# Kernel tuning notes

Hardware: AMD Instinct MI355X
Metric: run time of the kernel (lower is better)

Reference implementation:

```python
import jax, jax.numpy as jnp
import numpy as np

K = 16  # knn_k
LN_EPS = 1e-5


def _layernorm(x, g, b):
    mu = jnp.mean(x, axis=-1, keepdims=True)
    var = jnp.var(x, axis=-1, keepdims=True)
    return (x - mu) * jax.lax.rsqrt(var + LN_EPS) * g + b


def _mlp_block(x, W1, b1, g, be, W2, b2):
    # Linear -> LayerNorm -> GELU -> Linear (MLPBlock)
    h = x @ W1 + b1
    h = jax.nn.gelu(_layernorm(h, g, be))
    return h @ W2 + b2


def _knn(v):
    # v: [N,3] -> indices of K nearest neighbors [N,K] (self included, as in knn search)
    sq = jnp.sum(v * v, axis=-1)                       # [N]
    d = sq[:, None] + sq[None, :] - 2.0 * (v @ v.T)    # [N,N] squared dists
    return jax.lax.top_k(-d, K)[1]                     # [N,K]


def setup_inputs() -> dict:
    key = jax.random.key(0)
    ks = jax.random.split(key, 8)
    B, N, C_IN, C_OUT, HID = 2, 8192, 32, 64, 128
    E_IN = C_IN + C_IN + 3  # 67
    s = 0.02
    return {
        "vertices": jax.random.normal(ks[0], (B, N, 3), jnp.float32),
        "features": jax.random.normal(ks[1], (B, N, C_IN), jnp.float32),
        "W1": jax.random.normal(ks[2], (E_IN, HID), jnp.float32) * s,
        "b1": jnp.zeros((HID,), jnp.float32),
        "g1": jnp.ones((HID,), jnp.float32),
        "be1": jnp.zeros((HID,), jnp.float32),
        "W2": jax.random.normal(ks[3], (HID, C_OUT), jnp.float32) * s,
        "b2": jnp.zeros((C_OUT,), jnp.float32),
        "Wo1": jax.random.normal(ks[4], (C_OUT, HID), jnp.float32) * s,
        "bo1": jnp.zeros((HID,), jnp.float32),
        "go": jnp.ones((HID,), jnp.float32),
        "beo": jnp.zeros((HID,), jnp.float32),
        "Wo2": jax.random.normal(ks[5], (HID, C_OUT), jnp.float32) * s,
        "bo2": jnp.zeros((C_OUT,), jnp.float32),
    }


def reference(vertices, features, W1, b1, g1, be1, W2, b2,
              Wo1, bo1, go, beo, Wo2, bo2):
    # out_point_feature_type == 'same': output points == input points
    idx = jax.vmap(_knn)(vertices)                                   # [B,N,K]
    gather = jax.vmap(lambda a, i: jnp.take(a, i, axis=0))
    neigh_feat = gather(features, idx)                               # [B,N,K,C]
    neigh_vert = gather(vertices, idx)                               # [B,N,K,3]
    self_feat = jnp.broadcast_to(features[:, :, None, :], neigh_feat.shape)
    rel_pos = neigh_vert - vertices[:, :, None, :]                   # [B,N,K,3]
    edge = jnp.concatenate([neigh_feat, self_feat, rel_pos], axis=-1)  # [B,N,K,2C+3]
    edge = _mlp_block(edge, W1, b1, g1, be1, W2, b2)                 # [B,N,K,C_out]
    out = jnp.mean(edge, axis=2)                                     # 'mean' reduction over K neighbors
    out = _mlp_block(out, Wo1, bo1, go, beo, Wo2, bo2)               # [B,N,C_out]
    return out
```

## Files before the change

kernel.cpp:

```cpp
#include <hip/hip_runtime.h>
#include <hip/hip_bf16.h>
#include <math.h>

#define BATCH 2
#define NPTS  8192
#define CIN   32
#define HID   128
#define COUT  64
#define EIN   67
#define KNN   16

#define TILE  1024
#define CAP   128
#define CAP2  128

#define G      8
#define GROUPS 4
#define NBLK   (BATCH*NPTS/(G*GROUPS))

typedef unsigned short u16;
typedef unsigned long long u64;
typedef __attribute__((ext_vector_type(8))) short bf16x8;
typedef __attribute__((ext_vector_type(4))) float f32x4;

__device__ __forceinline__ u16 f2b(float f) {
    unsigned u = __float_as_uint(f);
    return (u16)((u + 0x7FFFu + ((u >> 16) & 1u)) >> 16);
}
__device__ __forceinline__ unsigned pk2(float a, float b) {
    return (unsigned)f2b(a) | ((unsigned)f2b(b) << 16);
}
__device__ __forceinline__ float gelu_t(float x) {
    float u = 1.5957691216057308f * (x + 0.044715f * x * x * x);
    float ex = __expf(u);
    return x * ex / (ex + 1.0f);
}

__global__ void prep_kernel(const float* __restrict__ verts, float4* __restrict__ pv) {
    int i = blockIdx.x * blockDim.x + threadIdx.x;
    if (i >= BATCH * NPTS) return;
    float x = verts[3 * i], y = verts[3 * i + 1], z = verts[3 * i + 2];
    float sq = __fadd_rn(__fadd_rn(__fmul_rn(x, x), __fmul_rn(y, y)), __fmul_rn(z, z));
    pv[i] = make_float4(x, y, z, sq);
}

__global__ __launch_bounds__(256, 4) void knn3_kernel(const float4* __restrict__ pv,
                                                      int* __restrict__ nbr_out_rows) {
    __shared__ float4 minv4[4][64];
    __shared__ float bufD[4][4][CAP2];
    __shared__ int   bufJ[4][4][CAP2];

    const int tid = threadIdx.x, lane = tid & 63, wv = tid >> 6;
    const int pt0 = (blockIdx.x * 4 + wv) * 4;
    const int b = pt0 >> 13, i0 = pt0 & (NPTS - 1);
    const float4* P = pv + (size_t)b * NPTS;

    float4 sp[4];
#pragma unroll
    for (int p = 0; p < 4; ++p) sp[p] = P[i0 + p];

    float mn[4] = {INFINITY, INFINITY, INFINITY, INFINITY};
#pragma unroll 4
    for (int t = 0; t < 64; ++t) {
        float4 c = P[t * 64 + lane];
#pragma unroll
        for (int p = 0; p < 4; ++p) {
            float dot = __fmul_rn(sp[p].x, c.x);
            dot = __fmaf_rn(sp[p].y, c.y, dot);
            dot = __fmaf_rn(sp[p].z, c.z, dot);
            float d = __fsub_rn(__fadd_rn(sp[p].w, c.w), __fmul_rn(2.0f, dot));
            mn[p] = fminf(mn[p], d);
        }
    }

    minv4[wv][lane] = make_float4(mn[0], mn[1], mn[2], mn[3]);
    __syncthreads();
    int rk[4] = {0, 0, 0, 0};
    for (int mm = 0; mm < 64; ++mm) {
        float4 v = minv4[wv][mm];
        rk[0] += (v.x < mn[0]) || (v.x == mn[0] && mm < lane);
        rk[1] += (v.y < mn[1]) || (v.y == mn[1] && mm < lane);
        rk[2] += (v.z < mn[2]) || (v.z == mn[2] && mm < lane);
        rk[3] += (v.w < mn[3]) || (v.w == mn[3] && mm < lane);
    }
    float tau[4];
#pragma unroll
    for (int p = 0; p < 4; ++p) {
        u64 bal = __ballot(rk[p] == 15);
        int srcl = __ffsll(bal) - 1;
        tau[p] = __shfl(mn[p], srcl, 64);
    }

    int base[4] = {0, 0, 0, 0};
#pragma unroll 2
    for (int t = 0; t < 128; ++t) {
        float4 c = P[t * 64 + lane];
        int j = t * 64 + lane;
#pragma unroll
        for (int p = 0; p < 4; ++p) {
            float dot = __fmul_rn(sp[p].x, c.x);
            dot = __fmaf_rn(sp[p].y, c.y, dot);
            dot = __fmaf_rn(sp[p].z, c.z, dot);
            float d = __fsub_rn(__fadd_rn(sp[p].w, c.w), __fmul_rn(2.0f, dot));
            bool pred = (d <= tau[p]);
            u64 mk = __ballot(pred);
            if (mk != 0ull) {
                if (pred) {
                    int pos = base[p] + (int)__popcll(mk & ((1ull << lane) - 1ull));
                    if (pos < CAP2) { bufD[wv][p][pos] = d; bufJ[wv][p][pos] = j; }
                }
                base[p] += (int)__popcll(mk);
            }
        }
    }

#pragma unroll
    for (int p = 0; p < 4; ++p) {
        int ns = (base[p] > CAP2) ? CAP2 : base[p];
        for (int slot = 0; slot < 2; ++slot) {
            int sidx = slot * 64 + lane;
            if (sidx < ns) {
                float ds = bufD[wv][p][sidx];
                int   js = bufJ[wv][p][sidx];
                int rank = 0;
                for (int mm = 0; mm < ns; ++mm) {
                    float dm = bufD[wv][p][mm];
                    int   jm = bufJ[wv][p][mm];
                    rank += (dm < ds) || (dm == ds && jm < js);
                }
                if (rank < KNN) nbr_out_rows[(size_t)(pt0 + p) * 64 + rank] = js;
            }
        }
    }
}

__global__ __launch_bounds__(256) void knn_kernel(const float* __restrict__ verts,
                                                  int* nbr_out_rows) {
    __shared__ float4 tilebuf[TILE];
    __shared__ float  bufD[4][CAP];
    __shared__ int    bufJ[4][CAP];

    const int tid = threadIdx.x, lane = tid & 63, wv = tid >> 6;
    const int pt = blockIdx.x * 4 + wv;
    const int b = pt >> 13, i = pt & (NPTS - 1);
    const float* vb = verts + (size_t)b * NPTS * 3;

    const float xi = vb[3 * i], yi = vb[3 * i + 1], zi = vb[3 * i + 2];
    const float sqi = __fadd_rn(__fadd_rn(__fmul_rn(xi, xi), __fmul_rn(yi, yi)),
                                __fmul_rn(zi, zi));

    float m_d = INFINITY;
    for (int t = 0; t < NPTS / TILE; ++t) {
        __syncthreads();
        for (int s = 0; s < TILE / 256; ++s) {
            int p = t * TILE + s * 256 + tid;
            float px = vb[3 * p], py = vb[3 * p + 1], pz = vb[3 * p + 2];
            float sq = __fadd_rn(__fadd_rn(__fmul_rn(px, px), __fmul_rn(py, py)),
                                 __fmul_rn(pz, pz));
            tilebuf[s * 256 + tid] = make_float4(px, py, pz, sq);
        }
        __syncthreads();
        for (int it = 0; it < TILE / 64; ++it) {
            float4 c = tilebuf[it * 64 + lane];
            float dot = __fmul_rn(xi, c.x);
            dot = __fmaf_rn(yi, c.y, dot);
            dot = __fmaf_rn(zi, c.z, dot);
            float d = __fsub_rn(__fadd_rn(sqi, c.w), __fmul_rn(2.0f, dot));
            m_d = fminf(m_d, d);
        }
    }
    __shared__ float minv[4][64];
    minv[wv][lane] = m_d;
    __syncthreads();
    int rnk = 0;
    for (int mm = 0; mm < 64; ++mm) {
        float vm = minv[wv][mm];
        rnk += (vm < m_d) || (vm == m_d && mm < lane);
    }
    u64 bal = __ballot(rnk == 15);
    float tau = __shfl(m_d, __ffsll(bal) - 1, 64);

    int base = 0;
    for (int t = 0; t < NPTS / TILE; ++t) {
        __syncthreads();
        for (int s = 0; s < TILE / 256; ++s) {
            int p = t * TILE + s * 256 + tid;
            float px = vb[3 * p], py = vb[3 * p + 1], pz = vb[3 * p + 2];
            float sq = __fadd_rn(__fadd_rn(__fmul_rn(px, px), __fmul_rn(py, py)),
                                 __fmul_rn(pz, pz));
            tilebuf[s * 256 + tid] = make_float4(px, py, pz, sq);
        }
        __syncthreads();
        for (int it = 0; it < TILE / 64; ++it) {
            int jl = it * 64 + lane;
            float4 c = tilebuf[jl];
            float dot = __fmul_rn(xi, c.x);
            dot = __fmaf_rn(yi, c.y, dot);
            dot = __fmaf_rn(zi, c.z, dot);
            float d = __fsub_rn(__fadd_rn(sqi, c.w), __fmul_rn(2.0f, dot));
            bool pred = (d <= tau);
            u64 mask = __ballot(pred);
            if (pred) {
                int pos = base + (int)__popcll(mask & ((1ull << lane) - 1ull));
                if (pos < CAP) { bufD[wv][pos] = d; bufJ[wv][pos] = t * TILE + jl; }
            }
            base += (int)__popcll(mask);
        }
    }
    int ns = (base > CAP) ? CAP : base;
    __syncthreads();
#pragma unroll
    for (int slot = 0; slot < 2; ++slot) {
        int sidx = slot * 64 + lane;
        if (sidx < ns) {
            float ds = bufD[wv][sidx];
            int   js = bufJ[wv][sidx];
            int rank = 0;
            for (int mm = 0; mm < ns; ++mm) {
                float dm = bufD[wv][mm];
                int   jm = bufJ[wv][mm];
                rank += (dm < ds) || (dm == ds && jm < js);
            }
            if (rank < KNN) nbr_out_rows[(size_t)pt * 64 + rank] = js;
        }
    }
}

__global__ __launch_bounds__(256, 2) void edge_kernel(
    const float* __restrict__ verts, const float* __restrict__ feats,
    const float* __restrict__ W1, const float* __restrict__ b1,
    const float* __restrict__ g1, const float* __restrict__ be1,
    const float* __restrict__ W2, const float* __restrict__ b2,
    const float* __restrict__ Wo1, const float* __restrict__ bo1,
    const float* __restrict__ go_, const float* __restrict__ beo,
    const float* __restrict__ Wo2, const float* __restrict__ bo2,
    float* out)
{
    __shared__ u16 EP[G][4][64][8];
    __shared__ u16 W1F[3][8][64][8];
    __shared__ float b1s[HID], g1s[HID], be1s[HID];
    __shared__ float b2s[COUT];
    __shared__ float meansh[32][68];
    __shared__ int   nbrs[G][KNN];

    const int tid  = threadIdx.x;
    const int lane = tid & 63, wv = tid >> 6;
    const int quad = lane >> 4, n16 = lane & 15;

    for (int s = tid; s < 3 * 8 * 64; s += 256) {
        int kt = s >> 9, nt = (s >> 6) & 7, ln = s & 63;
        int q = ln >> 4, nn = ln & 15;
        int col = nt * 16 + nn;
        union { bf16x8 v; unsigned u[4]; } pk;
#pragma unroll
        for (int jj = 0; jj < 4; ++jj) {
            int k0 = kt * 32 + q * 8 + jj * 2;
            float a  = (k0     < EIN) ? W1[(size_t)k0 * HID + col]       : 0.0f;
            float bq = (k0 + 1 < EIN) ? W1[(size_t)(k0 + 1) * HID + col] : 0.0f;
            pk.u[jj] = pk2(a, bq);
        }
        *(bf16x8*)&W1F[kt][nt][ln][0] = pk.v;
    }
    if (tid < HID) { b1s[tid] = b1[tid]; g1s[tid] = g1[tid]; be1s[tid] = be1[tid]; }
    if (tid < COUT) b2s[tid] = b2[tid];

    bf16x8 w2r[4][4];
#pragma unroll
    for (int kt2 = 0; kt2 < 4; ++kt2)
#pragma unroll
        for (int nt2 = 0; nt2 < 4; ++nt2) {
            union { bf16x8 v; unsigned u[4]; } pk;
#pragma unroll
            for (int jj = 0; jj < 4; ++jj) {
                int k0 = kt2 * 32 + quad * 8 + jj * 2;
                int o = nt2 * 16 + n16;
                pk.u[jj] = pk2(W2[(size_t)k0 * COUT + o],
                               W2[(size_t)(k0 + 1) * COUT + o]);
            }
            w2r[kt2][nt2] = pk.v;
        }

    for (int g = 0; g < GROUPS; ++g) {
        const int P0 = (blockIdx.x * GROUPS + g) * G;
        const int bb = P0 >> 13;
        const float* fb  = feats + (size_t)bb * NPTS * CIN;
        const float* vbk = verts + (size_t)bb * NPTS * 3;

        __syncthreads();
        if (tid < G * KNN)
            nbrs[tid >> 4][tid & 15] =
                ((const int*)out)[(size_t)(P0 + (tid >> 4)) * 64 + (tid & 15)];
        __syncthreads();

        {
            int m = tid & 127;
            int p = m >> 4, k = m & 15;
            int coff = tid >> 7;
            int jn = nbrs[p][k];
            int ip = (P0 & (NPTS - 1)) + p;
#pragma unroll
            for (int it = 0; it < 6; ++it) {
                int c8 = it * 2 + coff;
                union { bf16x8 v; unsigned u[4]; } pk;
                if (c8 < 4) {
                    const float* src = fb + (size_t)jn * CIN + c8 * 8;
                    float4 A = *(const float4*)src, B4 = *(const float4*)(src + 4);
                    pk.u[0] = pk2(A.x, A.y); pk.u[1] = pk2(A.z, A.w);
                    pk.u[2] = pk2(B4.x, B4.y); pk.u[3] = pk2(B4.z, B4.w);
                } else if (c8 < 8) {
                    const float* src = fb + (size_t)ip * CIN + (c8 - 4) * 8;
                    float4 A = *(const float4*)src, B4 = *(const float4*)(src + 4);
                    pk.u[0] = pk2(A.x, A.y); pk.u[1] = pk2(A.z, A.w);
                    pk.u[2] = pk2(B4.x, B4.y); pk.u[3] = pk2(B4.z, B4.w);
                } else if (c8 == 8) {
                    float dx = vbk[3 * jn]     - vbk[3 * ip];
                    float dy = vbk[3 * jn + 1] - vbk[3 * ip + 1];
                    float dz = vbk[3 * jn + 2] - vbk[3 * ip + 2];
                    pk.u[0] = pk2(dx, dy); pk.u[1] = pk2(dz, 0.0f);
                    pk.u[2] = 0u; pk.u[3] = 0u;
                } else {
                    pk.u[0] = pk.u[1] = pk.u[2] = pk.u[3] = 0u;
                }
                *(bf16x8*)&EP[p][c8 >> 2][k + 16 * (c8 & 3)][0] = pk.v;
            }
        }
        __syncthreads();

#pragma unroll
        for (int half = 0; half < 2; ++half) {
            const int mt = wv + half * 4;

            f32x4 acc[8];
#pragma unroll
            for (int nt = 0; nt < 8; ++nt) acc[nt] = (f32x4){0.f, 0.f, 0.f, 0.f};
#pragma unroll
            for (int kt = 0; kt < 3; ++kt) {
                bf16x8 a = *(bf16x8*)&EP[mt][kt][lane][0];
#pragma unroll
                for (int nt = 0; nt < 8; ++nt) {
                    bf16x8 bfr = *(bf16x8*)&W1F[kt][nt][lane][0];
                    acc[nt] = __builtin_amdgcn_mfma_f32_16x16x32_bf16(a, bfr, acc[nt], 0, 0, 0);
                }
            }

            float b1v[8], g1v[8], bev[8];
#pragma unroll
            for (int nt = 0; nt < 8; ++nt) {
                b1v[nt] = b1s[nt * 16 + n16];
                g1v[nt] = g1s[nt * 16 + n16];
                bev[nt] = be1s[nt * 16 + n16];
            }
            float s1[4] = {0,0,0,0}, s2[4] = {0,0,0,0};
#pragma unroll
            for (int nt = 0; nt < 8; ++nt)
#pragma unroll
                for (int r = 0; r < 4; ++r) {
                    float x = acc[nt][r] + b1v[nt];
                    s1[r] += x; s2[r] += x * x;
                }
#pragma unroll
            for (int r = 0; r < 4; ++r) {
#pragma unroll
                for (int off = 1; off < 16; off <<= 1) {
                    s1[r] += __shfl_xor(s1[r], off, 64);
                    s2[r] += __shfl_xor(s2[r], off, 64);
                }
            }
            float mu[4], rs[4];
#pragma unroll
            for (int r = 0; r < 4; ++r) {
                mu[r] = s1[r] * (1.0f / HID);
                float var = s2[r] * (1.0f / HID) - mu[r] * mu[r];
                rs[r] = rsqrtf(var + 1e-5f);
            }

#pragma unroll
            for (int nt = 0; nt < 8; ++nt) {
                int kt2 = nt >> 1;
                int q2  = (nt * 2 + (n16 >> 3)) & 3;
                int jj  = n16 & 7;
#pragma unroll
                for (int r = 0; r < 4; ++r) {
                    float x  = acc[nt][r] + b1v[nt];
                    float xn = (x - mu[r]) * rs[r] * g1v[nt] + bev[nt];
                    EP[mt][kt2][quad * 4 + r + 16 * q2][jj] = (u16)f2b(gelu_t(xn));
                }
            }

            f32x4 acc2[4];
#pragma unroll
            for (int nt2 = 0; nt2 < 4; ++nt2) acc2[nt2] = (f32x4){0.f, 0.f, 0.f, 0.f};
#pragma unroll
            for (int kt2 = 0; kt2 < 4; ++kt2) {
                bf16x8 a2 = *(bf16x8*)&EP[mt][kt2][lane][0];
#pragma unroll
                for (int nt2 = 0; nt2 < 4; ++nt2)
                    acc2[nt2] = __builtin_amdgcn_mfma_f32_16x16x32_bf16(a2, w2r[kt2][nt2], acc2[nt2], 0, 0, 0);
            }

#pragma unroll
            for (int nt2 = 0; nt2 < 4; ++nt2) {
                float cs = acc2[nt2][0] + acc2[nt2][1] + acc2[nt2][2] + acc2[nt2][3];
                cs += __shfl_xor(cs, 16, 64);
                cs += __shfl_xor(cs, 32, 64);
                if (quad == 0) {
                    int o = nt2 * 16 + n16;
                    meansh[g * 8 + mt][o] = cs * (1.0f / KNN) + b2s[o];
                }
            }
        }
    }

    __syncthreads();

    for (int s = tid; s < 2 * 8 * 64; s += 256) {
        int kt = s >> 9, nt = (s >> 6) & 7, ln = s & 63;
        int q = ln >> 4, nn = ln & 15;
        int col = nt * 16 + nn;
        union { bf16x8 v; unsigned u[4]; } pk;
#pragma unroll
        for (int jj = 0; jj < 4; ++jj) {
            int k0 = kt * 32 + q * 8 + jj * 2;
            pk.u[jj] = pk2(Wo1[(size_t)k0 * HID + col],
                           Wo1[(size_t)(k0 + 1) * HID + col]);
        }
        *(bf16x8*)&W1F[kt][nt][ln][0] = pk.v;
    }
    if (tid < HID) { b1s[tid] = bo1[tid]; g1s[tid] = go_[tid]; be1s[tid] = beo[tid]; }
    if (tid < COUT) b2s[tid] = bo2[tid];
#pragma unroll
    for (int kt2 = 0; kt2 < 4; ++kt2)
#pragma unroll
        for (int nt2 = 0; nt2 < 4; ++nt2) {
            union { bf16x8 v; unsigned u[4]; } pk;
#pragma unroll
            for (int jj = 0; jj < 4; ++jj) {
                int k0 = kt2 * 32 + quad * 8 + jj * 2;
                int o = nt2 * 16 + n16;
                pk.u[jj] = pk2(Wo2[(size_t)k0 * COUT + o],
                               Wo2[(size_t)(k0 + 1) * COUT + o]);
            }
            w2r[kt2][nt2] = pk.v;
        }
    __syncthreads();

    if (wv < 2) {
        const int tile = wv;

        bf16x8 af[2];
#pragma unroll
        for (int kt = 0; kt < 2; ++kt) {
            const float* mrow = &meansh[tile * 16 + n16][kt * 32 + quad * 8];
            float4 A = *(const float4*)mrow, B4 = *(const float4*)(mrow + 4);
            union { bf16x8 v; unsigned u[4]; } pk;
            pk.u[0] = pk2(A.x, A.y); pk.u[1] = pk2(A.z, A.w);
            pk.u[2] = pk2(B4.x, B4.y); pk.u[3] = pk2(B4.z, B4.w);
            af[kt] = pk.v;
        }

        f32x4 acc[8];
#pragma unroll
        for (int nt = 0; nt < 8; ++nt) acc[nt] = (f32x4){0.f, 0.f, 0.f, 0.f};
#pragma unroll
        for (int kt = 0; kt < 2; ++kt)
#pragma unroll
            for (int nt = 0; nt < 8; ++nt) {
                bf16x8 bfr = *(bf16x8*)&W1F[kt][nt][lane][0];
                acc[nt] = __builtin_amdgcn_mfma_f32_16x16x32_bf16(af[kt], bfr, acc[nt], 0, 0, 0);
            }

        float b1v[8], g1v[8], bev[8];
#pragma unroll
        for (int nt = 0; nt < 8; ++nt) {
            b1v[nt] = b1s[nt * 16 + n16];
            g1v[nt] = g1s[nt * 16 + n16];
            bev[nt] = be1s[nt * 16 + n16];
        }
        float s1[4] = {0,0,0,0}, s2[4] = {0,0,0,0};
#pragma unroll
        for (int nt = 0; nt < 8; ++nt)
#pragma unroll
            for (int r = 0; r < 4; ++r) {
                float x = acc[nt][r] + b1v[nt];
                s1[r] += x; s2[r] += x * x;
            }
#pragma unroll
        for (int r = 0; r < 4; ++r) {
#pragma unroll
            for (int off = 1; off < 16; off <<= 1) {
                s1[r] += __shfl_xor(s1[r], off, 64);
                s2[r] += __shfl_xor(s2[r], off, 64);
            }
        }
#pragma unroll
        for (int nt = 0; nt < 8; ++nt) {
            int kt2 = nt >> 1;
            int q2  = (nt * 2 + (n16 >> 3)) & 3;
            int jj  = n16 & 7;
#pragma unroll
            for (int r = 0; r < 4; ++r) {
                float mu = s1[r] * (1.0f / HID);
                float var = s2[r] * (1.0f / HID) - mu * mu;
                float rs = rsqrtf(var + 1e-5f);
                float x  = acc[nt][r] + b1v[nt];
                float xn = (x - mu) * rs * g1v[nt] + bev[nt];
                EP[tile][kt2][quad * 4 + r + 16 * q2][jj] = (u16)f2b(gelu_t(xn));
            }
        }

        f32x4 acc2[4];
#pragma unroll
        for (int nt2 = 0; nt2 < 4; ++nt2) acc2[nt2] = (f32x4){0.f, 0.f, 0.f, 0.f};
#pragma unroll
        for (int kt2 = 0; kt2 < 4; ++kt2) {
            bf16x8 a2 = *(bf16x8*)&EP[tile][kt2][lane][0];
#pragma unroll
            for (int nt2 = 0; nt2 < 4; ++nt2)
                acc2[nt2] = __builtin_amdgcn_mfma_f32_16x16x32_bf16(a2, w2r[kt2][nt2], acc2[nt2], 0, 0, 0);
        }

#pragma unroll
        for (int nt2 = 0; nt2 < 4; ++nt2) {
            int o = nt2 * 16 + n16;
#pragma unroll
            for (int r = 0; r < 4; ++r) {
                int ptl = blockIdx.x * 32 + tile * 16 + quad * 4 + r;
                out[(size_t)ptl * 64 + o] = acc2[nt2][r] + b2s[o];
            }
        }
    }
}

extern "C" void kernel_launch(void* const* d_in, const int* in_sizes, int n_in,
                              void* d_out, int out_size, void* d_ws, size_t ws_size,
                              hipStream_t stream) {
    const float* verts = (const float*)d_in[0];
    const float* feats = (const float*)d_in[1];
    const float* W1  = (const float*)d_in[2];
    const float* b1  = (const float*)d_in[3];
    const float* g1  = (const float*)d_in[4];
    const float* be1 = (const float*)d_in[5];
    const float* W2  = (const float*)d_in[6];
    const float* b2  = (const float*)d_in[7];
    const float* Wo1 = (const float*)d_in[8];
    const float* bo1 = (const float*)d_in[9];
    const float* go_ = (const float*)d_in[10];
    const float* beo = (const float*)d_in[11];
    const float* Wo2 = (const float*)d_in[12];
    const float* bo2 = (const float*)d_in[13];
    float* out = (float*)d_out;

    (void)in_sizes; (void)n_in; (void)out_size;

    const size_t pv_bytes = (size_t)BATCH * NPTS * sizeof(float4);
    if (ws_size >= pv_bytes) {
        float4* pv = (float4*)d_ws;
        prep_kernel<<<(BATCH * NPTS + 255) / 256, 256, 0, stream>>>(verts, pv);
        knn3_kernel<<<(BATCH * NPTS) / 16, 256, 0, stream>>>(pv, (int*)out);
    } else {
        knn_kernel<<<(BATCH * NPTS) / 4, 256, 0, stream>>>(verts, (int*)out);
    }
    edge_kernel<<<NBLK, 256, 0, stream>>>(
        verts, feats, W1, b1, g1, be1, W2, b2,
        Wo1, bo1, go_, beo, Wo2, bo2, out);
}
```

Before: 229.0 us.

## Rework KNN to 8 queries per wave and per-wave edge MLP pipeline

The KNN kernel now handles 8 query points per wave and uses a folded FMA form of the distance (-2x·c + |c|^2) with a small margin on the threshold. Candidates are collected through LDS atomics, and exact distances are recomputed only for the selected candidates. The edge kernel is restructured so each wave processes its own 4 points with software-prefetched register loads, replacing block-wide shared gather and sync, and the grid now uses 16 points per block. This trades more KNN registers and lower occupancy, plus nondeterministic candidate order, for less ALU work per distance and fewer barriers.

```diff
diff --git a/kernel.cpp b/kernel.cpp
--- a/kernel.cpp
+++ b/kernel.cpp
@@ -12,11 +12,8 @@
 
 #define TILE  1024
 #define CAP   128
-#define CAP2  128
-
-#define G      8
-#define GROUPS 4
-#define NBLK   (BATCH*NPTS/(G*GROUPS))
+#define KPTS  8
+#define KMARGIN 1e-3f
 
 typedef unsigned short u16;
 typedef unsigned long long u64;
@@ -44,93 +41,109 @@
     pv[i] = make_float4(x, y, z, sq);
 }
 
-__global__ __launch_bounds__(256, 4) void knn3_kernel(const float4* __restrict__ pv,
+__global__ __launch_bounds__(256, 3) void knn4_kernel(const float4* __restrict__ pv,
                                                       int* __restrict__ nbr_out_rows) {
-    __shared__ float4 minv4[4][64];
-    __shared__ float bufD[4][4][CAP2];
-    __shared__ int   bufJ[4][4][CAP2];
+    __shared__ int   bufJ[4][KPTS][CAP];
+    __shared__ float bufD[4][KPTS][CAP];
+    __shared__ int   cnt[4][KPTS];
+    __shared__ float4 mA[4][64], mB[4][64];
 
     const int tid = threadIdx.x, lane = tid & 63, wv = tid >> 6;
-    const int pt0 = (blockIdx.x * 4 + wv) * 4;
+    const int pt0 = (blockIdx.x * 4 + wv) * KPTS;
     const int b = pt0 >> 13, i0 = pt0 & (NPTS - 1);
     const float4* P = pv + (size_t)b * NPTS;
 
-    float4 sp[4];
-#pragma unroll
-    for (int p = 0; p < 4; ++p) sp[p] = P[i0 + p];
-
-    float mn[4] = {INFINITY, INFINITY, INFINITY, INFINITY};
+    float4 sp[KPTS];
+    float ax[KPTS], ay[KPTS], az[KPTS];
+#pragma unroll
+    for (int p = 0; p < KPTS; ++p) {
+        sp[p] = P[i0 + p];
+        ax[p] = -2.0f * sp[p].x; ay[p] = -2.0f * sp[p].y; az[p] = -2.0f * sp[p].z;
+    }
+    if (lane < KPTS) cnt[wv][lane] = 0;
+
+    float mn[KPTS];
+#pragma unroll
+    for (int p = 0; p < KPTS; ++p) mn[p] = INFINITY;
 #pragma unroll 4
     for (int t = 0; t < 64; ++t) {
         float4 c = P[t * 64 + lane];
 #pragma unroll
-        for (int p = 0; p < 4; ++p) {
+        for (int p = 0; p < KPTS; ++p) {
+            float f = __fmaf_rn(ax[p], c.x,
+                      __fmaf_rn(ay[p], c.y,
+                      __fmaf_rn(az[p], c.z, c.w)));
+            mn[p] = fminf(mn[p], f);
+        }
+    }
+
+    mA[wv][lane] = make_float4(mn[0], mn[1], mn[2], mn[3]);
+    mB[wv][lane] = make_float4(mn[4], mn[5], mn[6], mn[7]);
+    int rk[KPTS];
+#pragma unroll
+    for (int p = 0; p < KPTS; ++p) rk[p] = 0;
+    for (int mm = 0; mm < 64; ++mm) {
+        float4 a = mA[wv][mm], bq = mB[wv][mm];
+        rk[0] += (a.x < mn[0]) || (a.x == mn[0] && mm < lane);
+        rk[1] += (a.y < mn[1]) || (a.y == mn[1] && mm < lane);
+        rk[2] += (a.z < mn[2]) || (a.z == mn[2] && mm < lane);
+        rk[3] += (a.w < mn[3]) || (a.w == mn[3] && mm < lane);
+        rk[4] += (bq.x < mn[4]) || (bq.x == mn[4] && mm < lane);
+        rk[5] += (bq.y < mn[5]) || (bq.y == mn[5] && mm < lane);
+        rk[6] += (bq.z < mn[6]) || (bq.z == mn[6] && mm < lane);
+        rk[7] += (bq.w < mn[7]) || (bq.w == mn[7] && mm < lane);
+    }
+    float tp[KPTS];
+#pragma unroll
+    for (int p = 0; p < KPTS; ++p) {
+        u64 bal = __ballot(rk[p] == 15);
+        int srcl = __ffsll(bal) - 1;
+        tp[p] = __shfl(mn[p], srcl, 64) + KMARGIN;
+    }
+
+#pragma unroll 2
+    for (int t = 0; t < 128; ++t) {
+        float4 c = P[t * 64 + lane];
+        int j = t * 64 + lane;
+#pragma unroll
+        for (int p = 0; p < KPTS; ++p) {
+            float f = __fmaf_rn(ax[p], c.x,
+                      __fmaf_rn(ay[p], c.y,
+                      __fmaf_rn(az[p], c.z, c.w)));
+            if (f <= tp[p]) {
+                int pos = atomicAdd(&cnt[wv][p], 1);
+                if (pos < CAP) bufJ[wv][p][pos] = j;
+            }
+        }
+    }
+
+#pragma unroll
+    for (int p = 0; p < KPTS; ++p) {
+        int ns = cnt[wv][p]; ns = (ns > CAP) ? CAP : ns;
+        float dloc[2]; int jloc[2];
+#pragma unroll
+        for (int slot = 0; slot < 2; ++slot) {
+            int sidx = slot * 64 + lane;
+            bool act = sidx < ns;
+            int js = act ? bufJ[wv][p][sidx] : 0;
+            float4 c = P[js];
             float dot = __fmul_rn(sp[p].x, c.x);
             dot = __fmaf_rn(sp[p].y, c.y, dot);
             dot = __fmaf_rn(sp[p].z, c.z, dot);
             float d = __fsub_rn(__fadd_rn(sp[p].w, c.w), __fmul_rn(2.0f, dot));
-            mn[p] = fminf(mn[p], d);
-        }
-    }
-
-    minv4[wv][lane] = make_float4(mn[0], mn[1], mn[2], mn[3]);
-    __syncthreads();
-    int rk[4] = {0, 0, 0, 0};
-    for (int mm = 0; mm < 64; ++mm) {
-        float4 v = minv4[wv][mm];
-        rk[0] += (v.x < mn[0]) || (v.x == mn[0] && mm < lane);
-        rk[1] += (v.y < mn[1]) || (v.y == mn[1] && mm < lane);
-        rk[2] += (v.z < mn[2]) || (v.z == mn[2] && mm < lane);
-        rk[3] += (v.w < mn[3]) || (v.w == mn[3] && mm < lane);
-    }
-    float tau[4];
-#pragma unroll
-    for (int p = 0; p < 4; ++p) {
-        u64 bal = __ballot(rk[p] == 15);
-        int srcl = __ffsll(bal) - 1;
-        tau[p] = __shfl(mn[p], srcl, 64);
-    }
-
-    int base[4] = {0, 0, 0, 0};
-#pragma unroll 2
-    for (int t = 0; t < 128; ++t) {
-        float4 c = P[t * 64 + lane];
-        int j = t * 64 + lane;
-#pragma unroll
-        for (int p = 0; p < 4; ++p) {
-            float dot = __fmul_rn(sp[p].x, c.x);
-            dot = __fmaf_rn(sp[p].y, c.y, dot);
-            dot = __fmaf_rn(sp[p].z, c.z, dot);
-            float d = __fsub_rn(__fadd_rn(sp[p].w, c.w), __fmul_rn(2.0f, dot));
-            bool pred = (d <= tau[p]);
-            u64 mk = __ballot(pred);
-            if (mk != 0ull) {
-                if (pred) {
-                    int pos = base[p] + (int)__popcll(mk & ((1ull << lane) - 1ull));
-                    if (pos < CAP2) { bufD[wv][p][pos] = d; bufJ[wv][p][pos] = j; }
-                }
-                base[p] += (int)__popcll(mk);
-            }
-        }
-    }
-
-#pragma unroll
-    for (int p = 0; p < 4; ++p) {
-        int ns = (base[p] > CAP2) ? CAP2 : base[p];
-        for (int slot = 0; slot < 2; ++slot) {
-            int sidx = slot * 64 + lane;
-            if (sidx < ns) {
-                float ds = bufD[wv][p][sidx];
-                int   js = bufJ[wv][p][sidx];
-                int rank = 0;
-                for (int mm = 0; mm < ns; ++mm) {
-                    float dm = bufD[wv][p][mm];
-                    int   jm = bufJ[wv][p][mm];
-                    rank += (dm < ds) || (dm == ds && jm < js);
-                }
-                if (rank < KNN) nbr_out_rows[(size_t)(pt0 + p) * 64 + rank] = js;
-            }
-        }
+            if (act) bufD[wv][p][sidx] = d;
+            dloc[slot] = d; jloc[slot] = js;
+        }
+        int r0 = 0, r1 = 0;
+        for (int mm = 0; mm < ns; ++mm) {
+            float dm = bufD[wv][p][mm]; int jm = bufJ[wv][p][mm];
+            r0 += (dm < dloc[0]) || (dm == dloc[0] && jm < jloc[0]);
+            r1 += (dm < dloc[1]) || (dm == dloc[1] && jm < jloc[1]);
+        }
+        if (lane < ns && r0 < KNN)
+            nbr_out_rows[(size_t)(pt0 + p) * 64 + r0] = jloc[0];
+        if (64 + lane < ns && r1 < KNN)
+            nbr_out_rows[(size_t)(pt0 + p) * 64 + r1] = jloc[1];
     }
 }
 
@@ -226,7 +239,7 @@
     }
 }
 
-__global__ __launch_bounds__(256, 2) void edge_kernel(
+__global__ __launch_bounds__(256, 3) void edge2_kernel(
     const float* __restrict__ verts, const float* __restrict__ feats,
     const float* __restrict__ W1, const float* __restrict__ b1,
     const float* __restrict__ g1, const float* __restrict__ be1,
@@ -236,12 +249,11 @@
     const float* __restrict__ Wo2, const float* __restrict__ bo2,
     float* out)
 {
-    __shared__ u16 EP[G][4][64][8];
+    __shared__ u16 EPw[4][4][64][8];
     __shared__ u16 W1F[3][8][64][8];
     __shared__ float b1s[HID], g1s[HID], be1s[HID];
     __shared__ float b2s[COUT];
-    __shared__ float meansh[32][68];
-    __shared__ int   nbrs[G][KNN];
+    __shared__ float meansh[16][68];
 
     const int tid  = threadIdx.x;
     const int lane = tid & 63, wv = tid >> 6;
@@ -279,134 +291,146 @@
             }
             w2r[kt2][nt2] = pk.v;
         }
-
-    for (int g = 0; g < GROUPS; ++g) {
-        const int P0 = (blockIdx.x * GROUPS + g) * G;
-        const int bb = P0 >> 13;
-        const float* fb  = feats + (size_t)bb * NPTS * CIN;
-        const float* vbk = verts + (size_t)bb * NPTS * 3;
-
-        __syncthreads();
-        if (tid < G * KNN)
-            nbrs[tid >> 4][tid & 15] =
-                ((const int*)out)[(size_t)(P0 + (tid >> 4)) * 64 + (tid & 15)];
-        __syncthreads();
+    __syncthreads();
+
+    const int ptb = blockIdx.x * 16;
+    const int bb  = ptb >> 13;
+    const float* fb  = feats + (size_t)bb * NPTS * CIN;
+    const float* vbk = verts + (size_t)bb * NPTS * 3;
+    const int ptw = ptb + wv * 4;
+    const int ipw = ptw & (NPTS - 1);
+
+    float b1v[8], g1v[8], bev[8];
+#pragma unroll
+    for (int nt = 0; nt < 8; ++nt) {
+        b1v[nt] = b1s[nt * 16 + n16];
+        g1v[nt] = g1s[nt * 16 + n16];
+        bev[nt] = be1s[nt * 16 + n16];
+    }
+
+    const int k16 = lane & 15;
+    const int qq  = lane >> 4;
+
+    int jnv[4];
+#pragma unroll
+    for (int pp = 0; pp < 4; ++pp)
+        jnv[pp] = ((const int*)out)[(size_t)(ptw + pp) * 64 + k16];
+
+    float4 nA[2], nB[2], sA[2], sB[2];
+    float rx[2], ry[2], rz[2];
+    {
+        const float* nsrc = fb + (size_t)jnv[0] * CIN + qq * 8;
+        nA[0] = *(const float4*)nsrc; nB[0] = *(const float4*)(nsrc + 4);
+        const float* ssrc = fb + (size_t)ipw * CIN + qq * 8;
+        sA[0] = *(const float4*)ssrc; sB[0] = *(const float4*)(ssrc + 4);
+        rx[0] = ry[0] = rz[0] = 0.0f;
+        if (qq == 0) {
+            int jn = jnv[0];
+            rx[0] = vbk[3 * jn]     - vbk[3 * ipw];
+            ry[0] = vbk[3 * jn + 1] - vbk[3 * ipw + 1];
+            rz[0] = vbk[3 * jn + 2] - vbk[3 * ipw + 2];
+        }
+    }
+
+#pragma unroll
+    for (int pp = 0; pp < 4; ++pp) {
+        const int cb = pp & 1, nb = cb ^ 1;
+        if (pp < 3) {
+            const float* nsrc = fb + (size_t)jnv[pp + 1] * CIN + qq * 8;
+            nA[nb] = *(const float4*)nsrc; nB[nb] = *(const float4*)(nsrc + 4);
+            const float* ssrc = fb + (size_t)(ipw + pp + 1) * CIN + qq * 8;
+            sA[nb] = *(const float4*)ssrc; sB[nb] = *(const float4*)(ssrc + 4);
+            rx[nb] = ry[nb] = rz[nb] = 0.0f;
+            if (qq == 0) {
+                int jn = jnv[pp + 1]; int ipn = ipw + pp + 1;
+                rx[nb] = vbk[3 * jn]     - vbk[3 * ipn];
+                ry[nb] = vbk[3 * jn + 1] - vbk[3 * ipn + 1];
+                rz[nb] = vbk[3 * jn + 2] - vbk[3 * ipn + 2];
+            }
+        }
 
         {
-            int m = tid & 127;
-            int p = m >> 4, k = m & 15;
-            int coff = tid >> 7;
-            int jn = nbrs[p][k];
-            int ip = (P0 & (NPTS - 1)) + p;
-#pragma unroll
-            for (int it = 0; it < 6; ++it) {
-                int c8 = it * 2 + coff;
-                union { bf16x8 v; unsigned u[4]; } pk;
-                if (c8 < 4) {
-                    const float* src = fb + (size_t)jn * CIN + c8 * 8;
-                    float4 A = *(const float4*)src, B4 = *(const float4*)(src + 4);
-                    pk.u[0] = pk2(A.x, A.y); pk.u[1] = pk2(A.z, A.w);
-                    pk.u[2] = pk2(B4.x, B4.y); pk.u[3] = pk2(B4.z, B4.w);
-                } else if (c8 < 8) {
-                    const float* src = fb + (size_t)ip * CIN + (c8 - 4) * 8;
-                    float4 A = *(const float4*)src, B4 = *(const float4*)(src + 4);
-                    pk.u[0] = pk2(A.x, A.y); pk.u[1] = pk2(A.z, A.w);
-                    pk.u[2] = pk2(B4.x, B4.y); pk.u[3] = pk2(B4.z, B4.w);
-                } else if (c8 == 8) {
-                    float dx = vbk[3 * jn]     - vbk[3 * ip];
-                    float dy = vbk[3 * jn + 1] - vbk[3 * ip + 1];
-                    float dz = vbk[3 * jn + 2] - vbk[3 * ip + 2];
-                    pk.u[0] = pk2(dx, dy); pk.u[1] = pk2(dz, 0.0f);
-                    pk.u[2] = 0u; pk.u[3] = 0u;
-                } else {
-                    pk.u[0] = pk.u[1] = pk.u[2] = pk.u[3] = 0u;
-                }
-                *(bf16x8*)&EP[p][c8 >> 2][k + 16 * (c8 & 3)][0] = pk.v;
-            }
-        }
-        __syncthreads();
-
-#pragma unroll
-        for (int half = 0; half < 2; ++half) {
-            const int mt = wv + half * 4;
-
-            f32x4 acc[8];
-#pragma unroll
-            for (int nt = 0; nt < 8; ++nt) acc[nt] = (f32x4){0.f, 0.f, 0.f, 0.f};
-#pragma unroll
-            for (int kt = 0; kt < 3; ++kt) {
-                bf16x8 a = *(bf16x8*)&EP[mt][kt][lane][0];
-#pragma unroll
-                for (int nt = 0; nt < 8; ++nt) {
-                    bf16x8 bfr = *(bf16x8*)&W1F[kt][nt][lane][0];
-                    acc[nt] = __builtin_amdgcn_mfma_f32_16x16x32_bf16(a, bfr, acc[nt], 0, 0, 0);
-                }
-            }
-
-            float b1v[8], g1v[8], bev[8];
+            union { bf16x8 v; unsigned u[4]; } e0, e1, e2;
+            e0.u[0] = pk2(nA[cb].x, nA[cb].y); e0.u[1] = pk2(nA[cb].z, nA[cb].w);
+            e0.u[2] = pk2(nB[cb].x, nB[cb].y); e0.u[3] = pk2(nB[cb].z, nB[cb].w);
+            e1.u[0] = pk2(sA[cb].x, sA[cb].y); e1.u[1] = pk2(sA[cb].z, sA[cb].w);
+            e1.u[2] = pk2(sB[cb].x, sB[cb].y); e1.u[3] = pk2(sB[cb].z, sB[cb].w);
+            e2.u[0] = e2.u[1] = e2.u[2] = e2.u[3] = 0u;
+            if (qq == 0) { e2.u[0] = pk2(rx[cb], ry[cb]); e2.u[1] = pk2(rz[cb], 0.0f); }
+            *(bf16x8*)&EPw[wv][0][lane][0] = e0.v;
+            *(bf16x8*)&EPw[wv][1][lane][0] = e1.v;
+            *(bf16x8*)&EPw[wv][2][lane][0] = e2.v;
+        }
+
+        f32x4 acc[8];
+#pragma unroll
+        for (int nt = 0; nt < 8; ++nt) acc[nt] = (f32x4){0.f, 0.f, 0.f, 0.f};
+#pragma unroll
+        for (int kt = 0; kt < 3; ++kt) {
+            bf16x8 a = *(bf16x8*)&EPw[wv][kt][lane][0];
 #pragma unroll
             for (int nt = 0; nt < 8; ++nt) {
-                b1v[nt] = b1s[nt * 16 + n16];
-                g1v[nt] = g1s[nt * 16 + n16];
-                bev[nt] = be1s[nt * 16 + n16];
-            }
-            float s1[4] = {0,0,0,0}, s2[4] = {0,0,0,0};
-#pragma unroll
-            for (int nt = 0; nt < 8; ++nt)
-#pragma unroll
-                for (int r = 0; r < 4; ++r) {
-                    float x = acc[nt][r] + b1v[nt];
-                    s1[r] += x; s2[r] += x * x;
-                }
+                bf16x8 bfr = *(bf16x8*)&W1F[kt][nt][lane][0];
+                acc[nt] = __builtin_amdgcn_mfma_f32_16x16x32_bf16(a, bfr, acc[nt], 0, 0, 0);
+            }
+        }
+
+        float s1[4] = {0,0,0,0}, s2[4] = {0,0,0,0};
+#pragma unroll
+        for (int nt = 0; nt < 8; ++nt)
 #pragma unroll
             for (int r = 0; r < 4; ++r) {
-#pragma unroll
-                for (int off = 1; off < 16; off <<= 1) {
-                    s1[r] += __shfl_xor(s1[r], off, 64);
-                    s2[r] += __shfl_xor(s2[r], off, 64);
-                }
-            }
-            float mu[4], rs[4];
+                float x = acc[nt][r] + b1v[nt];
+                s1[r] += x; s2[r] += x * x;
+            }
+#pragma unroll
+        for (int r = 0; r < 4; ++r) {
+#pragma unroll
+            for (int off = 1; off < 16; off <<= 1) {
+                s1[r] += __shfl_xor(s1[r], off, 64);
+                s2[r] += __shfl_xor(s2[r], off, 64);
+            }
+        }
+        float mu[4], rs[4];
+#pragma unroll
+        for (int r = 0; r < 4; ++r) {
+            mu[r] = s1[r] * (1.0f / HID);
+            float var = s2[r] * (1.0f / HID) - mu[r] * mu[r];
+            rs[r] = rsqrtf(var + 1e-5f);
+        }
+
+#pragma unroll
+        for (int nt = 0; nt < 8; ++nt) {
+            int kt2 = nt >> 1;
+            int q2  = (nt * 2 + (n16 >> 3)) & 3;
+            int jj  = n16 & 7;
 #pragma unroll
             for (int r = 0; r < 4; ++r) {
-                mu[r] = s1[r] * (1.0f / HID);
-                float var = s2[r] * (1.0f / HID) - mu[r] * mu[r];
-                rs[r] = rsqrtf(var + 1e-5f);
-            }
-
-#pragma unroll
-            for (int nt = 0; nt < 8; ++nt) {
-                int kt2 = nt >> 1;
-                int q2  = (nt * 2 + (n16 >> 3)) & 3;
-                int jj  = n16 & 7;
-#pragma unroll
-                for (int r = 0; r < 4; ++r) {
-                    float x  = acc[nt][r] + b1v[nt];
-                    float xn = (x - mu[r]) * rs[r] * g1v[nt] + bev[nt];
-                    EP[mt][kt2][quad * 4 + r + 16 * q2][jj] = (u16)f2b(gelu_t(xn));
-                }
-            }
-
-            f32x4 acc2[4];
-#pragma unroll
-            for (int nt2 = 0; nt2 < 4; ++nt2) acc2[nt2] = (f32x4){0.f, 0.f, 0.f, 0.f};
-#pragma unroll
-            for (int kt2 = 0; kt2 < 4; ++kt2) {
-                bf16x8 a2 = *(bf16x8*)&EP[mt][kt2][lane][0];
-#pragma unroll
-                for (int nt2 = 0; nt2 < 4; ++nt2)
-                    acc2[nt2] = __builtin_amdgcn_mfma_f32_16x16x32_bf16(a2, w2r[kt2][nt2], acc2[nt2], 0, 0, 0);
-            }
-
-#pragma unroll
-            for (int nt2 = 0; nt2 < 4; ++nt2) {
-                float cs = acc2[nt2][0] + acc2[nt2][1] + acc2[nt2][2] + acc2[nt2][3];
-                cs += __shfl_xor(cs, 16, 64);
-                cs += __shfl_xor(cs, 32, 64);
-                if (quad == 0) {
-                    int o = nt2 * 16 + n16;
-                    meansh[g * 8 + mt][o] = cs * (1.0f / KNN) + b2s[o];
-                }
+                float x  = acc[nt][r] + b1v[nt];
+                float xn = (x - mu[r]) * rs[r] * g1v[nt] + bev[nt];
+                EPw[wv][kt2][quad * 4 + r + 16 * q2][jj] = (u16)f2b(gelu_t(xn));
+            }
+        }
+
+        f32x4 acc2[4];
+#pragma unroll
+        for (int nt2 = 0; nt2 < 4; ++nt2) acc2[nt2] = (f32x4){0.f, 0.f, 0.f, 0.f};
+#pragma unroll
+        for (int kt2 = 0; kt2 < 4; ++kt2) {
+            bf16x8 a2 = *(bf16x8*)&EPw[wv][kt2][lane][0];
+#pragma unroll
+            for (int nt2 = 0; nt2 < 4; ++nt2)
+                acc2[nt2] = __builtin_amdgcn_mfma_f32_16x16x32_bf16(a2, w2r[kt2][nt2], acc2[nt2], 0, 0, 0);
+        }
+
+#pragma unroll
+        for (int nt2 = 0; nt2 < 4; ++nt2) {
+            float cs = acc2[nt2][0] + acc2[nt2][1] + acc2[nt2][2] + acc2[nt2][3];
+            cs += __shfl_xor(cs, 16, 64);
+            cs += __shfl_xor(cs, 32, 64);
+            if (quad == 0) {
+                int o = nt2 * 16 + n16;
+                meansh[wv * 4 + pp][o] = cs * (1.0f / KNN) + b2s[o];
             }
         }
     }
@@ -444,13 +468,11 @@
         }
     __syncthreads();
 
-    if (wv < 2) {
-        const int tile = wv;
-
+    if (wv == 0) {
         bf16x8 af[2];
 #pragma unroll
         for (int kt = 0; kt < 2; ++kt) {
-            const float* mrow = &meansh[tile * 16 + n16][kt * 32 + quad * 8];
+            const float* mrow = &meansh[n16][kt * 32 + quad * 8];
             float4 A = *(const float4*)mrow, B4 = *(const float4*)(mrow + 4);
             union { bf16x8 v; unsigned u[4]; } pk;
             pk.u[0] = pk2(A.x, A.y); pk.u[1] = pk2(A.z, A.w);
@@ -469,19 +491,19 @@
                 acc[nt] = __builtin_amdgcn_mfma_f32_16x16x32_bf16(af[kt], bfr, acc[nt], 0, 0, 0);
             }
 
-        float b1v[8], g1v[8], bev[8];
+        float pb1[8], pg1[8], pbe[8];
 #pragma unroll
         for (int nt = 0; nt < 8; ++nt) {
-            b1v[nt] = b1s[nt * 16 + n16];
-            g1v[nt] = g1s[nt * 16 + n16];
-            bev[nt] = be1s[nt * 16 + n16];
+            pb1[nt] = b1s[nt * 16 + n16];
+            pg1[nt] = g1s[nt * 16 + n16];
+            pbe[nt] = be1s[nt * 16 + n16];
         }
         float s1[4] = {0,0,0,0}, s2[4] = {0,0,0,0};
 #pragma unroll
         for (int nt = 0; nt < 8; ++nt)
 #pragma unroll
             for (int r = 0; r < 4; ++r) {
-                float x = acc[nt][r] + b1v[nt];
+                float x = acc[nt][r] + pb1[nt];
                 s1[r] += x; s2[r] += x * x;
             }
 #pragma unroll
@@ -502,9 +524,9 @@
                 float mu = s1[r] * (1.0f / HID);
                 float var = s2[r] * (1.0f / HID) - mu * mu;
                 float rs = rsqrtf(var + 1e-5f);
-                float x  = acc[nt][r] + b1v[nt];
-                float xn = (x - mu) * rs * g1v[nt] + bev[nt];
-                EP[tile][kt2][quad * 4 + r + 16 * q2][jj] = (u16)f2b(gelu_t(xn));
+                float x  = acc[nt][r] + pb1[nt];
+                float xn = (x - mu) * rs * pg1[nt] + pbe[nt];
+                EPw[0][kt2][quad * 4 + r + 16 * q2][jj] = (u16)f2b(gelu_t(xn));
             }
         }
 
@@ -513,7 +535,7 @@
         for (int nt2 = 0; nt2 < 4; ++nt2) acc2[nt2] = (f32x4){0.f, 0.f, 0.f, 0.f};
 #pragma unroll
         for (int kt2 = 0; kt2 < 4; ++kt2) {
-            bf16x8 a2 = *(bf16x8*)&EP[tile][kt2][lane][0];
+            bf16x8 a2 = *(bf16x8*)&EPw[0][kt2][lane][0];
 #pragma unroll
             for (int nt2 = 0; nt2 < 4; ++nt2)
                 acc2[nt2] = __builtin_amdgcn_mfma_f32_16x16x32_bf16(a2, w2r[kt2][nt2], acc2[nt2], 0, 0, 0);
@@ -524,7 +546,7 @@
             int o = nt2 * 16 + n16;
 #pragma unroll
             for (int r = 0; r < 4; ++r) {
-                int ptl = blockIdx.x * 32 + tile * 16 + quad * 4 + r;
+                int ptl = ptb + quad * 4 + r;
                 out[(size_t)ptl * 64 + o] = acc2[nt2][r] + b2s[o];
             }
         }
@@ -556,11 +578,11 @@
     if (ws_size >= pv_bytes) {
         float4* pv = (float4*)d_ws;
         prep_kernel<<<(BATCH * NPTS + 255) / 256, 256, 0, stream>>>(verts, pv);
-        knn3_kernel<<<(BATCH * NPTS) / 16, 256, 0, stream>>>(pv, (int*)out);
+        knn4_kernel<<<(BATCH * NPTS) / (4 * KPTS), 256, 0, stream>>>(pv, (int*)out);
     } else {
         knn_kernel<<<(BATCH * NPTS) / 4, 256, 0, stream>>>(verts, (int*)out);
     }
-    edge_kernel<<<NBLK, 256, 0, stream>>>(
+    edge2_kernel<<<(BATCH * NPTS) / 16, 256, 0, stream>>>(
         verts, feats, W1, b1, g1, be1, W2, b2,
         Wo1, bo1, go_, beo, Wo2, bo2, out);
 }
```

Result: slower. 310.7 us (+35.7%).
